# Optimization experiments

Measured on AMD Instinct MI355X. Metric: run time of the kernel, lower is better.

The kernel has to match this reference:

```python
import jax, jax.numpy as jnp
import numpy as np

ONE_WAY = False  # init kwarg: if False, messages flow both directions along each bond

def setup_inputs() -> dict:
    key = jax.random.key(0)
    k1, k2, k3, k4 = jax.random.split(key, 4)
    B, N, D, E = 32, 2048, 256, 1 << 20
    x = jax.random.normal(k1, (B, N, D), dtype=jnp.float32)
    batch_idx = jax.random.randint(k2, (E,), 0, B, dtype=jnp.int64)
    src_idx = jax.random.randint(k3, (E,), 0, N, dtype=jnp.int64)
    dst_idx = jax.random.randint(k4, (E,), 0, N, dtype=jnp.int64)
    return {"x": x, "batch_idx": batch_idx, "src_idx": src_idx, "dst_idx": dst_idx}

def reference(x, batch_idx, src_idx, dst_idx):
    B, N, D = x.shape
    x_flat = x.reshape(B * N, D)
    # flatten (batch, node) -> single segment id so one scatter-add covers all edges
    src = batch_idx * N + src_idx
    dst = batch_idx * N + dst_idx
    out = jnp.zeros_like(x_flat).at[dst].add(x_flat[src])
    if not ONE_WAY:
        out = out.at[src].add(x_flat[dst])
    out = out.reshape(B, N, D)
    return jnp.concatenate([out, x], axis=2)  # [B, N, 2D]
```

## Files before the change

### kernel.cpp

```cpp
#include <hip/hip_runtime.h>

#define NB   32
#define NN   2048
#define RTOT (NB * NN)
#define DIM  256
#define DIM2 512
#define CAP  128

#define EPT    4
#define NPASS  8
#define PSHIFT 13

#define BLKS_PER_BATCH (NN / 4)
#define GATHER_BLOCKS  (RTOT / 4)


typedef float vf4 __attribute__((ext_vector_type(4)));
typedef unsigned short vu4 __attribute__((ext_vector_type(4)));

__global__ __launch_bounds__(256) void zero_counts(int* __restrict__ c) {
    int i = blockIdx.x * 256 + threadIdx.x;
    if (i < RTOT) c[i] = 0;
}

__global__ __launch_bounds__(256) void convert_bf16(const float* __restrict__ x,
                                                    unsigned short* __restrict__ xb) {
    const int NT = 2048 * 256;
    int t = blockIdx.x * 256 + threadIdx.x;
    const vf4* x4 = (const vf4*)x;
    vu4* b4 = (vu4*)xb;
    for (int i = t; i < RTOT * DIM / 4; i += NT) {
        vf4 v = x4[i];
        vu4 o;
#pragma unroll
        for (int k = 0; k < 4; ++k) {
            unsigned u = __float_as_uint(v[k]);
            unsigned r = u + 0x7fffu + ((u >> 16) & 1u);
            o[k] = (unsigned short)(r >> 16);
        }
        b4[i] = o;
    }
}

__global__ __launch_bounds__(256) void fill_buckets(const int* __restrict__ b,
                                                    const int* __restrict__ s,
                                                    const int* __restrict__ d,
                                                    int* __restrict__ cnt,
                                                    unsigned short* __restrict__ bucket,
                                                    int E) {
    int t = blockIdx.x * 256 + threadIdx.x;
    int base = t * EPT;

    int rs[EPT], rd[EPT];

    if (base + EPT <= E) {
        int4 b4 = ((const int4*)b)[t];
        int4 s4 = ((const int4*)s)[t];
        int4 d4 = ((const int4*)d)[t];
        rs[0] = b4.x * NN + s4.x;  rd[0] = b4.x * NN + d4.x;
        rs[1] = b4.y * NN + s4.y;  rd[1] = b4.y * NN + d4.y;
        rs[2] = b4.z * NN + s4.z;  rd[2] = b4.z * NN + d4.z;
        rs[3] = b4.w * NN + s4.w;  rd[3] = b4.w * NN + d4.w;
    } else {
#pragma unroll
        for (int i = 0; i < EPT; ++i) {
            int e = base + i;
            if (e < E) {
                int bb = b[e];
                rs[i] = bb * NN + s[e];
                rd[i] = bb * NN + d[e];
            } else {
                rs[i] = -1;
                rd[i] = -1;
            }
        }
    }

    for (int p = 0; p < NPASS; ++p) {
#pragma unroll
        for (int i = 0; i < EPT; ++i) {
            if ((rs[i] >> PSHIFT) == p) {
                int q = atomicAdd(&cnt[rs[i]], 1);
                if (q < CAP) bucket[(long)rs[i] * CAP + q] = (unsigned short)rd[i];
            }
            if ((rd[i] >> PSHIFT) == p) {
                int q = atomicAdd(&cnt[rd[i]], 1);
                if (q < CAP) bucket[(long)rd[i] * CAP + q] = (unsigned short)rs[i];
            }
        }
    }
}

__device__ inline vf4 bf16x4_to_f32(uint2 q) {
    vf4 v;
    v[0] = __uint_as_float(q.x << 16);
    v[1] = __uint_as_float(q.x & 0xffff0000u);
    v[2] = __uint_as_float(q.y << 16);
    v[3] = __uint_as_float(q.y & 0xffff0000u);
    return v;
}

__global__ __launch_bounds__(256) void gather_bf16(const float* __restrict__ x,
                                                   const unsigned short* __restrict__ xb,
                                                   const int* __restrict__ cnt,
                                                   const unsigned short* __restrict__ bucket,
                                                   float* __restrict__ out) {
    int p = blockIdx.x;
    int l;
    if (gridDim.x == GATHER_BLOCKS) {
        int xcd = p & 7;
        int u   = p >> 3;
        int bat = xcd + 8 * (u >> 9);
        l = bat * BLKS_PER_BATCH + (u & (BLKS_PER_BATCH - 1));
    } else {
        l = p;
    }

    int lane = threadIdx.x & 63;
    int row = __builtin_amdgcn_readfirstlane((l << 2) + (threadIdx.x >> 6));
    if (row >= RTOT) return;

    int n = __builtin_amdgcn_readfirstlane(cnt[row]);
    if (n > CAP) n = CAP;
    const unsigned* l32 = (const unsigned*)(bucket + (size_t)row * CAP);

    const uint2* xb2 = (const uint2*)xb;
    const vf4*   x4  = (const vf4*)x;
    vf4 xown = x4[((size_t)row << 6) + lane];

    vf4 acc0 = (vf4){0.f,0.f,0.f,0.f};
    vf4 acc1 = (vf4){0.f,0.f,0.f,0.f};
    vf4 acc2 = (vf4){0.f,0.f,0.f,0.f};
    vf4 acc3 = (vf4){0.f,0.f,0.f,0.f};

    int j = 0;
    for (; j + 8 <= n; j += 8) {
        int k = j >> 1;
        unsigned w0 = l32[k + 0];
        unsigned w1 = l32[k + 1];
        unsigned w2 = l32[k + 2];
        unsigned w3 = l32[k + 3];
        unsigned r0 = w0 & 0xffffu, r1 = w0 >> 16;
        unsigned r2 = w1 & 0xffffu, r3 = w1 >> 16;
        unsigned r4 = w2 & 0xffffu, r5 = w2 >> 16;
        unsigned r6 = w3 & 0xffffu, r7 = w3 >> 16;
        uint2 a0 = xb2[(size_t)((r0 << 6) + lane)];
        uint2 a1 = xb2[(size_t)((r1 << 6) + lane)];
        uint2 a2 = xb2[(size_t)((r2 << 6) + lane)];
        uint2 a3 = xb2[(size_t)((r3 << 6) + lane)];
        uint2 a4 = xb2[(size_t)((r4 << 6) + lane)];
        uint2 a5 = xb2[(size_t)((r5 << 6) + lane)];
        uint2 a6 = xb2[(size_t)((r6 << 6) + lane)];
        uint2 a7 = xb2[(size_t)((r7 << 6) + lane)];
        acc0 += bf16x4_to_f32(a0); acc1 += bf16x4_to_f32(a1);
        acc2 += bf16x4_to_f32(a2); acc3 += bf16x4_to_f32(a3);
        acc0 += bf16x4_to_f32(a4); acc1 += bf16x4_to_f32(a5);
        acc2 += bf16x4_to_f32(a6); acc3 += bf16x4_to_f32(a7);
    }
    for (; j + 4 <= n; j += 4) {
        int k = j >> 1;
        unsigned w0 = l32[k + 0];
        unsigned w1 = l32[k + 1];
        unsigned r0 = w0 & 0xffffu, r1 = w0 >> 16;
        unsigned r2 = w1 & 0xffffu, r3 = w1 >> 16;
        uint2 a0 = xb2[(size_t)((r0 << 6) + lane)];
        uint2 a1 = xb2[(size_t)((r1 << 6) + lane)];
        uint2 a2 = xb2[(size_t)((r2 << 6) + lane)];
        uint2 a3 = xb2[(size_t)((r3 << 6) + lane)];
        acc0 += bf16x4_to_f32(a0); acc1 += bf16x4_to_f32(a1);
        acc2 += bf16x4_to_f32(a2); acc3 += bf16x4_to_f32(a3);
    }
    for (; j < n; ++j) {
        unsigned w0 = l32[j >> 1];
        unsigned r = (j & 1) ? (w0 >> 16) : (w0 & 0xffffu);
        uint2 a = xb2[(size_t)((r << 6) + lane)];
        acc0 += bf16x4_to_f32(a);
    }

    vf4 acc = (acc0 + acc1) + (acc2 + acc3);

    vf4* o = (vf4*)(out + (size_t)row * DIM2);
    __builtin_nontemporal_store(acc,  &o[lane]);
    __builtin_nontemporal_store(xown, &o[64 + lane]);
}

__global__ __launch_bounds__(256) void gather_f32(const float* __restrict__ x,
                                                  const int* __restrict__ cnt,
                                                  const unsigned short* __restrict__ bucket,
                                                  float* __restrict__ out) {
    int p = blockIdx.x;
    int l;
    if (gridDim.x == GATHER_BLOCKS) {
        int xcd = p & 7;
        int u   = p >> 3;
        int bat = xcd + 8 * (u >> 9);
        l = bat * BLKS_PER_BATCH + (u & (BLKS_PER_BATCH - 1));
    } else {
        l = p;
    }
    int lane = threadIdx.x & 63;
    int row = __builtin_amdgcn_readfirstlane((l << 2) + (threadIdx.x >> 6));
    if (row >= RTOT) return;
    int n = __builtin_amdgcn_readfirstlane(cnt[row]);
    if (n > CAP) n = CAP;
    const unsigned* l32 = (const unsigned*)(bucket + (size_t)row * CAP);
    const vf4* x4 = (const vf4*)x;
    vf4 xown = x4[((size_t)row << 6) + lane];
    vf4 acc0 = (vf4){0.f,0.f,0.f,0.f};
    vf4 acc1 = (vf4){0.f,0.f,0.f,0.f};
    vf4 acc2 = (vf4){0.f,0.f,0.f,0.f};
    vf4 acc3 = (vf4){0.f,0.f,0.f,0.f};
    int j = 0;
    for (; j + 8 <= n; j += 8) {
        int k = j >> 1;
        unsigned w0 = l32[k+0], w1 = l32[k+1], w2 = l32[k+2], w3 = l32[k+3];
        unsigned r0 = w0 & 0xffffu, r1 = w0 >> 16;
        unsigned r2 = w1 & 0xffffu, r3 = w1 >> 16;
        unsigned r4 = w2 & 0xffffu, r5 = w2 >> 16;
        unsigned r6 = w3 & 0xffffu, r7 = w3 >> 16;
        vf4 a0 = x4[(size_t)((r0 << 6) + lane)];
        vf4 a1 = x4[(size_t)((r1 << 6) + lane)];
        vf4 a2 = x4[(size_t)((r2 << 6) + lane)];
        vf4 a3 = x4[(size_t)((r3 << 6) + lane)];
        vf4 a4 = x4[(size_t)((r4 << 6) + lane)];
        vf4 a5 = x4[(size_t)((r5 << 6) + lane)];
        vf4 a6 = x4[(size_t)((r6 << 6) + lane)];
        vf4 a7 = x4[(size_t)((r7 << 6) + lane)];
        acc0 += a0; acc1 += a1; acc2 += a2; acc3 += a3;
        acc0 += a4; acc1 += a5; acc2 += a6; acc3 += a7;
    }
    for (; j + 4 <= n; j += 4) {
        int k = j >> 1;
        unsigned w0 = l32[k+0], w1 = l32[k+1];
        unsigned r0 = w0 & 0xffffu, r1 = w0 >> 16;
        unsigned r2 = w1 & 0xffffu, r3 = w1 >> 16;
        vf4 a0 = x4[(size_t)((r0 << 6) + lane)];
        vf4 a1 = x4[(size_t)((r1 << 6) + lane)];
        vf4 a2 = x4[(size_t)((r2 << 6) + lane)];
        vf4 a3 = x4[(size_t)((r3 << 6) + lane)];
        acc0 += a0; acc1 += a1; acc2 += a2; acc3 += a3;
    }
    for (; j < n; ++j) {
        unsigned w0 = l32[j >> 1];
        unsigned r = (j & 1) ? (w0 >> 16) : (w0 & 0xffffu);
        acc0 += x4[(size_t)((r << 6) + lane)];
    }
    vf4 acc = (acc0 + acc1) + (acc2 + acc3);
    vf4* o = (vf4*)(out + (size_t)row * DIM2);
    __builtin_nontemporal_store(acc,  &o[lane]);
    __builtin_nontemporal_store(xown, &o[64 + lane]);
}

extern "C" void kernel_launch(void* const* d_in, const int* in_sizes, int n_in,
                              void* d_out, int out_size, void* d_ws, size_t ws_size,
                              hipStream_t stream) {
    const float* x         = (const float*)d_in[0];
    const int*   batch_idx = (const int*)d_in[1];
    const int*   src_idx   = (const int*)d_in[2];
    const int*   dst_idx   = (const int*)d_in[3];
    float*       out       = (float*)d_out;

    const int E = in_sizes[1];

    int* cnt = (int*)d_ws;
    unsigned short* bucket = (unsigned short*)(cnt + RTOT);
    unsigned short* xb = bucket + (size_t)RTOT * CAP;
    size_t need = (size_t)RTOT * 4 + (size_t)RTOT * CAP * 2 + (size_t)RTOT * DIM * 2;
    bool use_bf16 = (ws_size >= need);

    zero_counts<<<(RTOT + 255) / 256, 256, 0, stream>>>(cnt);
    if (use_bf16) {
        convert_bf16<<<2048, 256, 0, stream>>>(x, xb);
    }
    {
        int threads_needed = (E + EPT - 1) / EPT;
        int blocks = (threads_needed + 255) / 256;
        fill_buckets<<<blocks, 256, 0, stream>>>(batch_idx, src_idx, dst_idx,
                                                 cnt, bucket, E);
    }
    if (use_bf16) {
        gather_bf16<<<GATHER_BLOCKS, 256, 0, stream>>>(x, xb, cnt, bucket, out);
    } else {
        gather_f32<<<GATHER_BLOCKS, 256, 0, stream>>>(x, cnt, bucket, out);
    }
}
```

Baseline: 334.2 us.

## Fuse bf16 conversion into bucket fill kernel and gather two neighbors per wave

Merges the bf16 conversion kernel into the bucket-fill launch as extra blocks, so conversion and the atomic-heavy fill share one grid and can run concurrently. The gather kernel now splits each wave into two half-waves that each load 16-byte vectors from a different neighbor row, then combines the halves with a cross-half shuffle. This doubles the bytes per load instruction and halves the number of loop iterations over the neighbor list. The cost is the extra shuffle reduction and half the lanes sitting idle during the first output store.

```diff
diff --git a/kernel.cpp b/kernel.cpp
--- a/kernel.cpp
+++ b/kernel.cpp
@@ -10,6 +10,8 @@
 #define EPT    4
 #define NPASS  8
 #define PSHIFT 13
+#define CONV_BLOCKS   512
+#define CONV_PER_BLK  (RTOT * DIM / 4 / CONV_BLOCKS)
 
 #define BLKS_PER_BATCH (NN / 4)
 #define GATHER_BLOCKS  (RTOT / 4)
@@ -23,31 +25,42 @@
     if (i < RTOT) c[i] = 0;
 }
 
-__global__ __launch_bounds__(256) void convert_bf16(const float* __restrict__ x,
-                                                    unsigned short* __restrict__ xb) {
-    const int NT = 2048 * 256;
-    int t = blockIdx.x * 256 + threadIdx.x;
-    const vf4* x4 = (const vf4*)x;
-    vu4* b4 = (vu4*)xb;
-    for (int i = t; i < RTOT * DIM / 4; i += NT) {
-        vf4 v = x4[i];
-        vu4 o;
-#pragma unroll
-        for (int k = 0; k < 4; ++k) {
-            unsigned u = __float_as_uint(v[k]);
-            unsigned r = u + 0x7fffu + ((u >> 16) & 1u);
-            o[k] = (unsigned short)(r >> 16);
-        }
-        b4[i] = o;
-    }
-}
-
-__global__ __launch_bounds__(256) void fill_buckets(const int* __restrict__ b,
-                                                    const int* __restrict__ s,
-                                                    const int* __restrict__ d,
-                                                    int* __restrict__ cnt,
-                                                    unsigned short* __restrict__ bucket,
-                                                    int E) {
+__device__ inline vf4 bf16x4_to_f32(unsigned lo, unsigned hi) {
+    vf4 v;
+    v[0] = __uint_as_float(lo << 16);
+    v[1] = __uint_as_float(lo & 0xffff0000u);
+    v[2] = __uint_as_float(hi << 16);
+    v[3] = __uint_as_float(hi & 0xffff0000u);
+    return v;
+}
+
+__global__ __launch_bounds__(256) void fill_conv(const int* __restrict__ b,
+                                                 const int* __restrict__ s,
+                                                 const int* __restrict__ d,
+                                                 int* __restrict__ cnt,
+                                                 unsigned short* __restrict__ bucket,
+                                                 const float* __restrict__ x,
+                                                 unsigned short* __restrict__ xb,
+                                                 int E, int fillBlocks) {
+    if ((int)blockIdx.x >= fillBlocks) {
+        int cb = blockIdx.x - fillBlocks;
+        const vf4* x4 = (const vf4*)x;
+        vu4* o4 = (vu4*)xb;
+        int beg = cb * CONV_PER_BLK;
+        for (int i = beg + (int)threadIdx.x; i < beg + CONV_PER_BLK; i += 256) {
+            vf4 v = x4[i];
+            vu4 o;
+#pragma unroll
+            for (int k = 0; k < 4; ++k) {
+                unsigned u = __float_as_uint(v[k]);
+                unsigned r = u + 0x7fffu + ((u >> 16) & 1u);
+                o[k] = (unsigned short)(r >> 16);
+            }
+            o4[i] = o;
+        }
+        return;
+    }
+
     int t = blockIdx.x * 256 + threadIdx.x;
     int base = t * EPT;
 
@@ -89,15 +102,6 @@
             }
         }
     }
-}
-
-__device__ inline vf4 bf16x4_to_f32(uint2 q) {
-    vf4 v;
-    v[0] = __uint_as_float(q.x << 16);
-    v[1] = __uint_as_float(q.x & 0xffff0000u);
-    v[2] = __uint_as_float(q.y << 16);
-    v[3] = __uint_as_float(q.y & 0xffff0000u);
-    return v;
 }
 
 __global__ __launch_bounds__(256) void gather_bf16(const float* __restrict__ x,
@@ -117,6 +121,8 @@
     }
 
     int lane = threadIdx.x & 63;
+    int half = lane >> 5;
+    int sub  = lane & 31;
     int row = __builtin_amdgcn_readfirstlane((l << 2) + (threadIdx.x >> 6));
     if (row >= RTOT) return;
 
@@ -124,63 +130,63 @@
     if (n > CAP) n = CAP;
     const unsigned* l32 = (const unsigned*)(bucket + (size_t)row * CAP);
 
-    const uint2* xb2 = (const uint2*)xb;
+    const uint4* xb4 = (const uint4*)xb;
     const vf4*   x4  = (const vf4*)x;
     vf4 xown = x4[((size_t)row << 6) + lane];
 
-    vf4 acc0 = (vf4){0.f,0.f,0.f,0.f};
-    vf4 acc1 = (vf4){0.f,0.f,0.f,0.f};
-    vf4 acc2 = (vf4){0.f,0.f,0.f,0.f};
-    vf4 acc3 = (vf4){0.f,0.f,0.f,0.f};
-
+    vf4 aA0 = (vf4){0.f,0.f,0.f,0.f};
+    vf4 aB0 = (vf4){0.f,0.f,0.f,0.f};
+    vf4 aA1 = (vf4){0.f,0.f,0.f,0.f};
+    vf4 aB1 = (vf4){0.f,0.f,0.f,0.f};
+
+    int pairs = n >> 1;
     int j = 0;
-    for (; j + 8 <= n; j += 8) {
-        int k = j >> 1;
-        unsigned w0 = l32[k + 0];
-        unsigned w1 = l32[k + 1];
-        unsigned w2 = l32[k + 2];
-        unsigned w3 = l32[k + 3];
-        unsigned r0 = w0 & 0xffffu, r1 = w0 >> 16;
-        unsigned r2 = w1 & 0xffffu, r3 = w1 >> 16;
-        unsigned r4 = w2 & 0xffffu, r5 = w2 >> 16;
-        unsigned r6 = w3 & 0xffffu, r7 = w3 >> 16;
-        uint2 a0 = xb2[(size_t)((r0 << 6) + lane)];
-        uint2 a1 = xb2[(size_t)((r1 << 6) + lane)];
-        uint2 a2 = xb2[(size_t)((r2 << 6) + lane)];
-        uint2 a3 = xb2[(size_t)((r3 << 6) + lane)];
-        uint2 a4 = xb2[(size_t)((r4 << 6) + lane)];
-        uint2 a5 = xb2[(size_t)((r5 << 6) + lane)];
-        uint2 a6 = xb2[(size_t)((r6 << 6) + lane)];
-        uint2 a7 = xb2[(size_t)((r7 << 6) + lane)];
-        acc0 += bf16x4_to_f32(a0); acc1 += bf16x4_to_f32(a1);
-        acc2 += bf16x4_to_f32(a2); acc3 += bf16x4_to_f32(a3);
-        acc0 += bf16x4_to_f32(a4); acc1 += bf16x4_to_f32(a5);
-        acc2 += bf16x4_to_f32(a6); acc3 += bf16x4_to_f32(a7);
-    }
-    for (; j + 4 <= n; j += 4) {
-        int k = j >> 1;
-        unsigned w0 = l32[k + 0];
-        unsigned w1 = l32[k + 1];
-        unsigned r0 = w0 & 0xffffu, r1 = w0 >> 16;
-        unsigned r2 = w1 & 0xffffu, r3 = w1 >> 16;
-        uint2 a0 = xb2[(size_t)((r0 << 6) + lane)];
-        uint2 a1 = xb2[(size_t)((r1 << 6) + lane)];
-        uint2 a2 = xb2[(size_t)((r2 << 6) + lane)];
-        uint2 a3 = xb2[(size_t)((r3 << 6) + lane)];
-        acc0 += bf16x4_to_f32(a0); acc1 += bf16x4_to_f32(a1);
-        acc2 += bf16x4_to_f32(a2); acc3 += bf16x4_to_f32(a3);
-    }
-    for (; j < n; ++j) {
-        unsigned w0 = l32[j >> 1];
-        unsigned r = (j & 1) ? (w0 >> 16) : (w0 & 0xffffu);
-        uint2 a = xb2[(size_t)((r << 6) + lane)];
-        acc0 += bf16x4_to_f32(a);
-    }
-
-    vf4 acc = (acc0 + acc1) + (acc2 + acc3);
+    for (; j + 4 <= pairs; j += 4) {
+        unsigned w0 = l32[j + 0];
+        unsigned w1 = l32[j + 1];
+        unsigned w2 = l32[j + 2];
+        unsigned w3 = l32[j + 3];
+        unsigned r0 = half ? (w0 >> 16) : (w0 & 0xffffu);
+        unsigned r1 = half ? (w1 >> 16) : (w1 & 0xffffu);
+        unsigned r2 = half ? (w2 >> 16) : (w2 & 0xffffu);
+        unsigned r3 = half ? (w3 >> 16) : (w3 & 0xffffu);
+        uint4 q0 = xb4[(size_t)((r0 << 5) + sub)];
+        uint4 q1 = xb4[(size_t)((r1 << 5) + sub)];
+        uint4 q2 = xb4[(size_t)((r2 << 5) + sub)];
+        uint4 q3 = xb4[(size_t)((r3 << 5) + sub)];
+        aA0 += bf16x4_to_f32(q0.x, q0.y); aB0 += bf16x4_to_f32(q0.z, q0.w);
+        aA1 += bf16x4_to_f32(q1.x, q1.y); aB1 += bf16x4_to_f32(q1.z, q1.w);
+        aA0 += bf16x4_to_f32(q2.x, q2.y); aB0 += bf16x4_to_f32(q2.z, q2.w);
+        aA1 += bf16x4_to_f32(q3.x, q3.y); aB1 += bf16x4_to_f32(q3.z, q3.w);
+    }
+    for (; j < pairs; ++j) {
+        unsigned w0 = l32[j];
+        unsigned r0 = half ? (w0 >> 16) : (w0 & 0xffffu);
+        uint4 q0 = xb4[(size_t)((r0 << 5) + sub)];
+        aA0 += bf16x4_to_f32(q0.x, q0.y); aB0 += bf16x4_to_f32(q0.z, q0.w);
+    }
+    if (n & 1) {
+        unsigned w0 = l32[pairs];
+        unsigned r0 = w0 & 0xffffu;
+        if (half == 0) {
+            uint4 q0 = xb4[(size_t)((r0 << 5) + sub)];
+            aA0 += bf16x4_to_f32(q0.x, q0.y); aB0 += bf16x4_to_f32(q0.z, q0.w);
+        }
+    }
+
+    vf4 aA = aA0 + aA1;
+    vf4 aB = aB0 + aB1;
+#pragma unroll
+    for (int k = 0; k < 4; ++k) {
+        aA[k] += __shfl_xor(aA[k], 32, 64);
+        aB[k] += __shfl_xor(aB[k], 32, 64);
+    }
 
     vf4* o = (vf4*)(out + (size_t)row * DIM2);
-    __builtin_nontemporal_store(acc,  &o[lane]);
+    if (half == 0) {
+        __builtin_nontemporal_store(aA, &o[2 * sub]);
+        __builtin_nontemporal_store(aB, &o[2 * sub + 1]);
+    }
     __builtin_nontemporal_store(xown, &o[64 + lane]);
 }
 
@@ -269,15 +275,13 @@
     bool use_bf16 = (ws_size >= need);
 
     zero_counts<<<(RTOT + 255) / 256, 256, 0, stream>>>(cnt);
-    if (use_bf16) {
-        convert_bf16<<<2048, 256, 0, stream>>>(x, xb);
-    }
-    {
-        int threads_needed = (E + EPT - 1) / EPT;
-        int blocks = (threads_needed + 255) / 256;
-        fill_buckets<<<blocks, 256, 0, stream>>>(batch_idx, src_idx, dst_idx,
-                                                 cnt, bucket, E);
-    }
+
+    int threads_needed = (E + EPT - 1) / EPT;
+    int fillBlocks = (threads_needed + 255) / 256;
+    int grid = fillBlocks + (use_bf16 ? CONV_BLOCKS : 0);
+    fill_conv<<<grid, 256, 0, stream>>>(batch_idx, src_idx, dst_idx,
+                                        cnt, bucket, x, xb, E, fillBlocks);
+
     if (use_bf16) {
         gather_bf16<<<GATHER_BLOCKS, 256, 0, stream>>>(x, xb, cnt, bucket, out);
     } else {
```

Result: faster. 296.8 us (-11.2%).
